# Performance work log

Hardware: AMD Instinct MI355X
Metric: run time of the kernel (lower is better)

Reference implementation:

```python
import jax, jax.numpy as jnp
import numpy as np

DIM = 128
EMB = 8
HID = 128
N = 50000
E = 400000
IN_DIM = 3 * DIM + EMB  # zi, zj, |zi-zj|, type_emb


def setup_inputs() -> dict:
    key = jax.random.key(0)
    ks = jax.random.split(key, 16)
    s = 0.05
    return {
        "z": jax.random.normal(ks[0], (N, DIM), dtype=jnp.float32),
        "edge_index": jax.random.randint(ks[1], (2, E), 0, N, dtype=jnp.int64),
        "edge_type": jax.random.randint(ks[2], (E,), 0, 2, dtype=jnp.int64),
        "type_emb": jax.random.normal(ks[3], (2, EMB), dtype=jnp.float32) * s,
        "ew1": jax.random.normal(ks[4], (IN_DIM, HID), dtype=jnp.float32) * s,
        "eb1": jnp.zeros((HID,), dtype=jnp.float32),
        "ew2": jax.random.normal(ks[5], (HID, 1), dtype=jnp.float32) * s,
        "eb2": jnp.zeros((1,), dtype=jnp.float32),
        "mw1": jax.random.normal(ks[6], (DIM, DIM), dtype=jnp.float32) * s,
        "mb1": jnp.zeros((DIM,), dtype=jnp.float32),
        "mw2": jax.random.normal(ks[7], (DIM, DIM), dtype=jnp.float32) * s,
        "mb2": jnp.zeros((DIM,), dtype=jnp.float32),
        "gamma": jnp.ones((DIM,), dtype=jnp.float32),
        "beta": jnp.zeros((DIM,), dtype=jnp.float32),
    }


def reference(z, edge_index, edge_type, type_emb, ew1, eb1, ew2, eb2,
              mw1, mb1, mw2, mb2, gamma, beta):
    src = edge_index[0]
    dst = edge_index[1]
    n = z.shape[0]

    # --- learn branch: edge MLP -> sigmoid -> segment softmax over src ---
    zi = z[src]              # [E, D]
    zj = z[dst]              # [E, D]
    te = type_emb[edge_type]  # [E, EMB]
    e_in = jnp.concatenate([zi, zj, jnp.abs(zi - zj), te], axis=1)  # [E, 3D+EMB]
    h = jax.nn.relu(e_in @ ew1 + eb1)
    w = jax.nn.sigmoid((h @ ew2 + eb2)[:, 0])  # [E]
    # scatter_reduce amax with include_self on a -1e9-filled buffer
    m = jax.ops.segment_max(w, src, num_segments=n)
    m = jnp.maximum(m, jnp.float32(-1e9))
    w_exp = jnp.exp(w - m[src])
    ssum = jax.ops.segment_sum(w_exp, src, num_segments=n)
    alpha_learned = w_exp / (ssum[src] + 1e-12)

    # --- uniform branch: alpha = 1/deg(src), msg MLP, scatter-add, LayerNorm ---
    deg = jax.ops.segment_sum(jnp.ones((src.shape[0],), z.dtype), src, num_segments=n)
    alpha_u = 1.0 / (deg[src] + 1e-12)
    msg = (jax.nn.relu(zj @ mw1 + mb1) @ mw2 + mb2) * alpha_u[:, None]  # [E, D]
    agg = jax.ops.segment_sum(msg, src, num_segments=n)  # [N, D]
    x = z + agg  # dropout inactive (eval mode)
    mu = jnp.mean(x, axis=-1, keepdims=True)
    var = jnp.mean(jnp.square(x - mu), axis=-1, keepdims=True)
    out = (x - mu) * jax.lax.rsqrt(var + 1e-5) * gamma + beta
    return (out, alpha_learned)
```

## Files before the change

kernel.cpp:

```cpp
#include <hip/hip_runtime.h>
#include <math.h>


typedef short bf16x8 __attribute__((ext_vector_type(8)));
typedef unsigned short ushort8 __attribute__((ext_vector_type(8)));
typedef float f32x4 __attribute__((ext_vector_type(4)));

__device__ inline short bf16_rne(float f) {
    unsigned u = __float_as_uint(f);
    u = (u + 0x7FFFu + ((u >> 16) & 1u)) >> 16;
    return (short)u;
}
__device__ inline float bf16_to_f(unsigned short h) {
    return __uint_as_float(((unsigned)h) << 16);
}

__global__ void prep_all(const float* __restrict__ te, const float* __restrict__ ew1,
                         const float* __restrict__ eb1, const float* __restrict__ mw1,
                         const float* __restrict__ mw2, float* __restrict__ T2,
                         unsigned short* __restrict__ Wap, unsigned short* __restrict__ Wbp,
                         unsigned short* __restrict__ Wcp, unsigned short* __restrict__ Mw1p,
                         unsigned short* __restrict__ Mw2p) {
    int b = blockIdx.x;
    if (b == 0) {
        int t = threadIdx.x;
        int row = t >> 7, j = t & 127;
        float s = eb1[j];
#pragma unroll
        for (int u = 0; u < 8; ++u) s += te[row * 8 + u] * ew1[(384 + u) * 128 + j];
        T2[row * 128 + j] = s;
        return;
    }
    const float* src = (b == 1) ? ew1 : (b == 2) ? ew1 + 128 * 128
                      : (b == 3) ? ew1 + 256 * 128 : (b == 4) ? mw1 : mw2;
    unsigned short* dst = (b == 1) ? Wap : (b == 2) ? Wbp
                         : (b == 3) ? Wcp : (b == 4) ? Mw1p : Mw2p;
    for (int idx = threadIdx.x; idx < 2048; idx += 256) {
        int ks = idx >> 9, ct = (idx >> 6) & 7, l = idx & 63;
        int kbase = ks * 32 + (l >> 4) * 8;
        int col = ct * 16 + (l & 15);
#pragma unroll
        for (int j = 0; j < 8; ++j)
            dst[(size_t)idx * 8 + j] =
                (unsigned short)bf16_rne(src[(size_t)(kbase + j) * 128 + col]);
    }
}

__global__ void deg_count(const int* __restrict__ ei, int* __restrict__ deg, int E) {
    int e = blockIdx.x * 256 + threadIdx.x;
    if (e >= E) return;
    atomicAdd(&deg[ei[e]], 1);
}

__global__ __launch_bounds__(256) void scan_local(const int* __restrict__ deg,
                                                  int* __restrict__ rowstart,
                                                  int* __restrict__ partials, int N) {
    __shared__ int wtot[4];
    int b = blockIdx.x, t = threadIdx.x, lane = t & 63, wid = t >> 6;
    int i0 = b * 1024 + t * 4;
    int v0 = (i0 + 0 < N) ? deg[i0 + 0] : 0;
    int v1 = (i0 + 1 < N) ? deg[i0 + 1] : 0;
    int v2 = (i0 + 2 < N) ? deg[i0 + 2] : 0;
    int v3 = (i0 + 3 < N) ? deg[i0 + 3] : 0;
    int ts = v0 + v1 + v2 + v3;
    int inc = ts;
#pragma unroll
    for (int off = 1; off < 64; off <<= 1) {
        int u = __shfl_up(inc, off);
        if (lane >= off) inc += u;
    }
    if (lane == 63) wtot[wid] = inc;
    __syncthreads();
    int woff = 0;
    if (wid > 0) woff += wtot[0];
    if (wid > 1) woff += wtot[1];
    if (wid > 2) woff += wtot[2];
    int excl = woff + inc - ts;
    if (i0 + 0 < N) rowstart[i0 + 0] = excl;
    if (i0 + 1 < N) rowstart[i0 + 1] = excl + v0;
    if (i0 + 2 < N) rowstart[i0 + 2] = excl + v0 + v1;
    if (i0 + 3 < N) rowstart[i0 + 3] = excl + v0 + v1 + v2;
    if (t == 255) partials[b] = woff + inc;
}

__global__ void scan_partials(int* __restrict__ partials, int nb) {
    int lane = threadIdx.x;
    int v = (lane < nb) ? partials[lane] : 0;
    int inc = v;
#pragma unroll
    for (int off = 1; off < 64; off <<= 1) {
        int u = __shfl_up(inc, off);
        if (lane >= off) inc += u;
    }
    if (lane < nb) partials[lane] = inc - v;
}

__global__ void scan_add(int* __restrict__ rowstart, const int* __restrict__ partials, int N) {
    int i = blockIdx.x * 256 + threadIdx.x;
    if (i < N) rowstart[i] += partials[i >> 10];
}

__global__ void place_edges(const int* __restrict__ ei, const int* __restrict__ etype,
                            int* __restrict__ cursor, const int* __restrict__ rowstart,
                            int4* __restrict__ cinfo, int E) {
    int e = blockIdx.x * 256 + threadIdx.x;
    if (e >= E) return;
    int s = ei[e], d = ei[E + e];
    int slot = rowstart[s] + atomicAdd(&cursor[s], 1);
    cinfo[slot] = make_int4(d, s, etype[e], e);
}

__global__ __launch_bounds__(256) void node_mfma(
        const void* __restrict__ Av, int a_bf16,
        const bf16x8* __restrict__ Bfr, const float* __restrict__ bias,
        void* __restrict__ Cv, int c_bf16, int relu, int M) {
    const int l = threadIdx.x & 63;
    const int wv = threadIdx.x >> 6;
    const int c = l & 15, g = l >> 4;
    const int row = blockIdx.x * 64 + wv * 16 + c;
    const int rowc = row < M ? row : M - 1;

    const float* af = (const float*)Av + (size_t)rowc * 128 + g * 8;
    const unsigned short* ah = (const unsigned short*)Av + (size_t)rowc * 128 + g * 8;

    f32x4 acc[8];
#pragma unroll
    for (int ct = 0; ct < 8; ++ct)
#pragma unroll
        for (int r = 0; r < 4; ++r) acc[ct][r] = 0.f;

#pragma unroll
    for (int ks = 0; ks < 4; ++ks) {
        bf16x8 a;
        if (a_bf16) {
            a = (bf16x8)(*(const ushort8*)(ah + ks * 32));
        } else {
            float4 x0 = *(const float4*)(af + ks * 32);
            float4 x1 = *(const float4*)(af + ks * 32 + 4);
            a[0] = bf16_rne(x0.x); a[1] = bf16_rne(x0.y);
            a[2] = bf16_rne(x0.z); a[3] = bf16_rne(x0.w);
            a[4] = bf16_rne(x1.x); a[5] = bf16_rne(x1.y);
            a[6] = bf16_rne(x1.z); a[7] = bf16_rne(x1.w);
        }
#pragma unroll
        for (int ct = 0; ct < 8; ++ct) {
            bf16x8 b = Bfr[(ks * 8 + ct) * 64 + l];
            acc[ct] = __builtin_amdgcn_mfma_f32_16x16x32_bf16(a, b, acc[ct], 0, 0, 0);
        }
    }

#pragma unroll
    for (int r = 0; r < 4; ++r) {
        int rr = blockIdx.x * 64 + wv * 16 + g * 4 + r;
        if (rr >= M) continue;
#pragma unroll
        for (int ct = 0; ct < 8; ++ct) {
            int j = ct * 16 + c;
            float v = acc[ct][r] + (bias ? bias[j] : 0.f);
            if (relu) v = fmaxf(v, 0.f);
            if (c_bf16)
                ((unsigned short*)Cv)[(size_t)rr * 128 + j] = (unsigned short)bf16_rne(v);
            else
                ((float*)Cv)[(size_t)rr * 128 + j] = v;
        }
    }
}

__global__ __launch_bounds__(256) void pa_pb_mfma(
        const float* __restrict__ z, const bf16x8* __restrict__ Ba,
        const bf16x8* __restrict__ Bb, float* __restrict__ Pa,
        float* __restrict__ Pb, unsigned short* __restrict__ zb16, int M) {
    const int l = threadIdx.x & 63;
    const int wv = threadIdx.x >> 6;
    const int c = l & 15, g = l >> 4;
    const int row = blockIdx.x * 64 + wv * 16 + c;
    const int rowc = row < M ? row : M - 1;
    const float* af = z + (size_t)rowc * 128 + g * 8;

    f32x4 acca[8], accb[8];
#pragma unroll
    for (int ct = 0; ct < 8; ++ct)
#pragma unroll
        for (int r = 0; r < 4; ++r) { acca[ct][r] = 0.f; accb[ct][r] = 0.f; }

#pragma unroll
    for (int ks = 0; ks < 4; ++ks) {
        float4 x0 = *(const float4*)(af + ks * 32);
        float4 x1 = *(const float4*)(af + ks * 32 + 4);
        bf16x8 a;
        a[0] = bf16_rne(x0.x); a[1] = bf16_rne(x0.y);
        a[2] = bf16_rne(x0.z); a[3] = bf16_rne(x0.w);
        a[4] = bf16_rne(x1.x); a[5] = bf16_rne(x1.y);
        a[6] = bf16_rne(x1.z); a[7] = bf16_rne(x1.w);
        if (row < M)
            *(ushort8*)(zb16 + (size_t)row * 128 + ks * 32 + g * 8) = (ushort8)a;
#pragma unroll
        for (int ct = 0; ct < 8; ++ct) {
            acca[ct] = __builtin_amdgcn_mfma_f32_16x16x32_bf16(
                a, Ba[(ks * 8 + ct) * 64 + l], acca[ct], 0, 0, 0);
            accb[ct] = __builtin_amdgcn_mfma_f32_16x16x32_bf16(
                a, Bb[(ks * 8 + ct) * 64 + l], accb[ct], 0, 0, 0);
        }
    }

#pragma unroll
    for (int r = 0; r < 4; ++r) {
        int rr = blockIdx.x * 64 + wv * 16 + g * 4 + r;
        if (rr >= M) continue;
#pragma unroll
        for (int ct = 0; ct < 8; ++ct) {
            int j = ct * 16 + c;
            Pa[(size_t)rr * 128 + j] = acca[ct][r];
            Pb[(size_t)rr * 128 + j] = accb[ct][r];
        }
    }
}

__global__ __launch_bounds__(256) void edge_mlp_mfma(
        const unsigned short* __restrict__ zb16, const int4* __restrict__ cinfo,
        const bf16x8* __restrict__ Bfr,
        const float* __restrict__ ew2, const float* __restrict__ eb2,
        const float* __restrict__ Pa, const float* __restrict__ Pb,
        const float* __restrict__ T2, float* __restrict__ expw,
        float* __restrict__ ssum, int E) {
    const int l = threadIdx.x & 63;
    const int wv = threadIdx.x >> 6;
    const int c = l & 15, g = l >> 4;
    const int slot0 = blockIdx.x * 64;

    const int ra = slot0 + wv * 16 + c;
    const int4 ciA = cinfo[ra];
    const unsigned short* zi = zb16 + (size_t)ciA.y * 128 + g * 8;
    const unsigned short* zj = zb16 + (size_t)ciA.x * 128 + g * 8;

    f32x4 acc[8];
#pragma unroll
    for (int ct = 0; ct < 8; ++ct)
#pragma unroll
        for (int r = 0; r < 4; ++r) acc[ct][r] = 0.f;

#pragma unroll
    for (int ks = 0; ks < 4; ++ks) {
        ushort8 ui = *(const ushort8*)(zi + ks * 32);
        ushort8 uj = *(const ushort8*)(zj + ks * 32);
        bf16x8 a;
#pragma unroll
        for (int k = 0; k < 8; ++k)
            a[k] = bf16_rne(fabsf(bf16_to_f(ui[k]) - bf16_to_f(uj[k])));
#pragma unroll
        for (int ct = 0; ct < 8; ++ct) {
            bf16x8 b = Bfr[(ks * 8 + ct) * 64 + l];
            acc[ct] = __builtin_amdgcn_mfma_f32_16x16x32_bf16(a, b, acc[ct], 0, 0, 0);
        }
    }

    const int eb = slot0 + wv * 16 + g * 4;
    int4 cr[4];
#pragma unroll
    for (int r = 0; r < 4; ++r) cr[r] = cinfo[eb + r];

    float s[4] = {0.f, 0.f, 0.f, 0.f};
#pragma unroll
    for (int ct = 0; ct < 8; ++ct) {
        int j = ct * 16 + c;
        float w2v = ew2[j];
#pragma unroll
        for (int r = 0; r < 4; ++r) {
            float h = acc[ct][r] + Pa[(size_t)cr[r].y * 128 + j]
                                 + Pb[(size_t)cr[r].x * 128 + j]
                                 + T2[cr[r].z * 128 + j];
            s[r] = fmaf(fmaxf(h, 0.f), w2v, s[r]);
        }
    }
#pragma unroll
    for (int r = 0; r < 4; ++r) {
        s[r] += __shfl_xor(s[r], 1);
        s[r] += __shfl_xor(s[r], 2);
        s[r] += __shfl_xor(s[r], 4);
        s[r] += __shfl_xor(s[r], 8);
    }
    if (c == 0) {
        const float eb2v = eb2[0];
#pragma unroll
        for (int r = 0; r < 4; ++r) {
            float w = 1.f / (1.f + expf(-(s[r] + eb2v)));
            float ewv = expf(w);
            expw[cr[r].w] = ewv;
            atomicAdd(&ssum[cr[r].y], ewv);
        }
    }
}

__global__ void alpha_k(const float* __restrict__ expw, const int* __restrict__ ei,
                        const float* __restrict__ ssum, float* __restrict__ oa, int E) {
    int e = blockIdx.x * 256 + threadIdx.x;
    if (e >= E) return;
    oa[e] = expw[e] / (ssum[ei[e]] + 1e-12f);
}

__global__ __launch_bounds__(256) void gather_ln(
        const float* __restrict__ z, const float* __restrict__ Mx,
        const int* __restrict__ rowstart, const int* __restrict__ deg,
        const int4* __restrict__ cinfo, const float* __restrict__ gamma,
        const float* __restrict__ beta, float* __restrict__ out, int N) {
    int wid = threadIdx.x >> 6, lane = threadIdx.x & 63;
    int n = blockIdx.x * 4 + wid;
    if (n >= N) return;
    int r0 = rowstart[n], dg = deg[n];
    float2 a0 = make_float2(0.f, 0.f), a1 = make_float2(0.f, 0.f);
    for (int c = 0; c < dg; c += 64) {
        int cnt = min(64, dg - c);
        int myd = (lane < cnt) ? cinfo[r0 + c + lane].x : 0;
        int j = 0;
        for (; j + 1 < cnt; j += 2) {
            int d0 = __shfl(myd, j), d1 = __shfl(myd, j + 1);
            float2 v0 = ((const float2*)(Mx + (size_t)d0 * 128))[lane];
            float2 v1 = ((const float2*)(Mx + (size_t)d1 * 128))[lane];
            a0.x += v0.x; a0.y += v0.y;
            a1.x += v1.x; a1.y += v1.y;
        }
        if (j < cnt) {
            int d0 = __shfl(myd, j);
            float2 v0 = ((const float2*)(Mx + (size_t)d0 * 128))[lane];
            a0.x += v0.x; a0.y += v0.y;
        }
    }
    float inv = 1.f / ((float)dg + 1e-12f);
    size_t base = (size_t)n * 128;
    float2 zz = ((const float2*)(z + base))[lane];
    float x0 = zz.x + (a0.x + a1.x) * inv;
    float x1 = zz.y + (a0.y + a1.y) * inv;
    float s = x0 + x1;
#pragma unroll
    for (int off = 1; off < 64; off <<= 1) s += __shfl_xor(s, off);
    float mu = s * (1.f / 128.f);
    float d0 = x0 - mu, d1 = x1 - mu;
    float v = d0 * d0 + d1 * d1;
#pragma unroll
    for (int off = 1; off < 64; off <<= 1) v += __shfl_xor(v, off);
    float rs = rsqrtf(v * (1.f / 128.f) + 1e-5f);
    float2 gg = ((const float2*)gamma)[lane];
    float2 bb = ((const float2*)beta)[lane];
    float2 o = make_float2(d0 * rs * gg.x + bb.x, d1 * rs * gg.y + bb.y);
    ((float2*)(out + base))[lane] = o;
}

extern "C" void kernel_launch(void* const* d_in, const int* in_sizes, int n_in,
                              void* d_out, int out_size, void* d_ws, size_t ws_size,
                              hipStream_t stream) {
    const float* z     = (const float*)d_in[0];
    const int*   ei    = (const int*)d_in[1];
    const int*   et    = (const int*)d_in[2];
    const float* temb  = (const float*)d_in[3];
    const float* ew1   = (const float*)d_in[4];
    const float* eb1   = (const float*)d_in[5];
    const float* ew2   = (const float*)d_in[6];
    const float* eb2   = (const float*)d_in[7];
    const float* mw1   = (const float*)d_in[8];
    const float* mb1   = (const float*)d_in[9];
    const float* mw2   = (const float*)d_in[10];
    const float* mb2   = (const float*)d_in[11];
    const float* gamma = (const float*)d_in[12];
    const float* beta  = (const float*)d_in[13];

    const int N = in_sizes[0] / 128;
    const int E = in_sizes[2];

    char* ws = (char*)d_ws;
    size_t off = 0;
    auto take = [&](size_t b) { char* p = ws + off; off += (b + 255) & ~(size_t)255; return p; };
    float*          Pa    = (float*)take((size_t)N * 128 * 4);
    float*          Pb    = (float*)take((size_t)N * 128 * 4);
    unsigned short* Hb    = (unsigned short*)take((size_t)N * 128 * 2);
    float*          Mx    = (float*)take((size_t)N * 128 * 4);
    unsigned short* zb16  = (unsigned short*)take((size_t)N * 128 * 2);
    char*           z0    = ws + off;
    float*          ssum  = (float*)take((size_t)N * 4);
    int*            deg   = (int*)take((size_t)N * 4);
    int*            cursor= (int*)take((size_t)N * 4);
    size_t          zb    = (size_t)((ws + off) - z0);
    int*            rowst = (int*)take((size_t)N * 4);
    int*            parts = (int*)take(256 * 4);
    int4*           cinfo = (int4*)take((size_t)E * 16);
    float*          expw  = (float*)take((size_t)E * 4);
    float*          T2    = (float*)take(2 * 128 * 4);
    unsigned short* Wap   = (unsigned short*)take(2048 * 8 * 2);
    unsigned short* Wbp   = (unsigned short*)take(2048 * 8 * 2);
    unsigned short* Wcp   = (unsigned short*)take(2048 * 8 * 2);
    unsigned short* Mw1p  = (unsigned short*)take(2048 * 8 * 2);
    unsigned short* Mw2p  = (unsigned short*)take(2048 * 8 * 2);

    float* out_x = (float*)d_out;
    float* out_a = out_x + (size_t)N * 128;

    hipMemsetAsync(z0, 0, zb, stream);
    prep_all<<<6, 256, 0, stream>>>(temb, ew1, eb1, mw1, mw2,
                                    T2, Wap, Wbp, Wcp, Mw1p, Mw2p);

    const int nb = (N + 1023) / 1024;
    deg_count<<<(E + 255) / 256, 256, 0, stream>>>(ei, deg, E);
    scan_local<<<nb, 256, 0, stream>>>(deg, rowst, parts, N);
    scan_partials<<<1, 64, 0, stream>>>(parts, nb);
    scan_add<<<(N + 255) / 256, 256, 0, stream>>>(rowst, parts, N);
    place_edges<<<(E + 255) / 256, 256, 0, stream>>>(ei, et, cursor, rowst, cinfo, E);

    int gb = (N + 63) / 64;
    pa_pb_mfma<<<gb, 256, 0, stream>>>(z, (const bf16x8*)Wap, (const bf16x8*)Wbp,
                                       Pa, Pb, zb16, N);
    node_mfma<<<gb, 256, 0, stream>>>(z, 0, (const bf16x8*)Mw1p, mb1,
                                      Hb, 1, 1, N);
    node_mfma<<<gb, 256, 0, stream>>>(Hb, 1, (const bf16x8*)Mw2p, mb2,
                                      Mx, 0, 0, N);

    edge_mlp_mfma<<<E / 64, 256, 0, stream>>>(zb16, cinfo, (const bf16x8*)Wcp, ew2, eb2,
                                              Pa, Pb, T2, expw, ssum, E);
    alpha_k<<<(E + 255) / 256, 256, 0, stream>>>(expw, ei, ssum, out_a, E);
    gather_ln<<<(N + 3) / 4, 256, 0, stream>>>(z, Mx, rowst, deg, cinfo, gamma, beta, out_x, N);
}
```

Measured before the change: 329.3 us.

## Fuse node projections and message MLP into one kernel, store Pa/Pb in bf16

Merges the Pa/Pb projection kernel and the two node MLP kernels into a single kernel. The z tile is converted to bf16 once, and the hidden activation goes through shared memory instead of a global bf16 buffer. Pa and Pb are now stored as bf16, which halves the bytes gathered per edge in the edge MLP. In exchange the fused kernel holds three accumulator sets, so register pressure rises and occupancy may drop, and the bf16 Pa/Pb add rounding error to the edge logits.

```diff
diff --git a/kernel.cpp b/kernel.cpp
--- a/kernel.cpp
+++ b/kernel.cpp
@@ -110,66 +110,14 @@
     cinfo[slot] = make_int4(d, s, etype[e], e);
 }
 
-__global__ __launch_bounds__(256) void node_mfma(
-        const void* __restrict__ Av, int a_bf16,
-        const bf16x8* __restrict__ Bfr, const float* __restrict__ bias,
-        void* __restrict__ Cv, int c_bf16, int relu, int M) {
-    const int l = threadIdx.x & 63;
-    const int wv = threadIdx.x >> 6;
-    const int c = l & 15, g = l >> 4;
-    const int row = blockIdx.x * 64 + wv * 16 + c;
-    const int rowc = row < M ? row : M - 1;
-
-    const float* af = (const float*)Av + (size_t)rowc * 128 + g * 8;
-    const unsigned short* ah = (const unsigned short*)Av + (size_t)rowc * 128 + g * 8;
-
-    f32x4 acc[8];
-#pragma unroll
-    for (int ct = 0; ct < 8; ++ct)
-#pragma unroll
-        for (int r = 0; r < 4; ++r) acc[ct][r] = 0.f;
-
-#pragma unroll
-    for (int ks = 0; ks < 4; ++ks) {
-        bf16x8 a;
-        if (a_bf16) {
-            a = (bf16x8)(*(const ushort8*)(ah + ks * 32));
-        } else {
-            float4 x0 = *(const float4*)(af + ks * 32);
-            float4 x1 = *(const float4*)(af + ks * 32 + 4);
-            a[0] = bf16_rne(x0.x); a[1] = bf16_rne(x0.y);
-            a[2] = bf16_rne(x0.z); a[3] = bf16_rne(x0.w);
-            a[4] = bf16_rne(x1.x); a[5] = bf16_rne(x1.y);
-            a[6] = bf16_rne(x1.z); a[7] = bf16_rne(x1.w);
-        }
-#pragma unroll
-        for (int ct = 0; ct < 8; ++ct) {
-            bf16x8 b = Bfr[(ks * 8 + ct) * 64 + l];
-            acc[ct] = __builtin_amdgcn_mfma_f32_16x16x32_bf16(a, b, acc[ct], 0, 0, 0);
-        }
-    }
-
-#pragma unroll
-    for (int r = 0; r < 4; ++r) {
-        int rr = blockIdx.x * 64 + wv * 16 + g * 4 + r;
-        if (rr >= M) continue;
-#pragma unroll
-        for (int ct = 0; ct < 8; ++ct) {
-            int j = ct * 16 + c;
-            float v = acc[ct][r] + (bias ? bias[j] : 0.f);
-            if (relu) v = fmaxf(v, 0.f);
-            if (c_bf16)
-                ((unsigned short*)Cv)[(size_t)rr * 128 + j] = (unsigned short)bf16_rne(v);
-            else
-                ((float*)Cv)[(size_t)rr * 128 + j] = v;
-        }
-    }
-}
-
-__global__ __launch_bounds__(256) void pa_pb_mfma(
+__global__ __launch_bounds__(256) void node_all(
         const float* __restrict__ z, const bf16x8* __restrict__ Ba,
-        const bf16x8* __restrict__ Bb, float* __restrict__ Pa,
-        float* __restrict__ Pb, unsigned short* __restrict__ zb16, int M) {
+        const bf16x8* __restrict__ Bb, const bf16x8* __restrict__ Bm1,
+        const bf16x8* __restrict__ Bm2, const float* __restrict__ mb1,
+        const float* __restrict__ mb2, unsigned short* __restrict__ Pa,
+        unsigned short* __restrict__ Pb, unsigned short* __restrict__ zb16,
+        float* __restrict__ Mx, int M) {
+    __shared__ unsigned short Hs[64][136];
     const int l = threadIdx.x & 63;
     const int wv = threadIdx.x >> 6;
     const int c = l & 15, g = l >> 4;
@@ -177,12 +125,13 @@
     const int rowc = row < M ? row : M - 1;
     const float* af = z + (size_t)rowc * 128 + g * 8;
 
-    f32x4 acca[8], accb[8];
+    f32x4 acca[8], accb[8], acch[8];
 #pragma unroll
     for (int ct = 0; ct < 8; ++ct)
 #pragma unroll
-        for (int r = 0; r < 4; ++r) { acca[ct][r] = 0.f; accb[ct][r] = 0.f; }
-
+        for (int r = 0; r < 4; ++r) { acca[ct][r] = 0.f; accb[ct][r] = 0.f; acch[ct][r] = 0.f; }
+
+    bf16x8 afrag[4];
 #pragma unroll
     for (int ks = 0; ks < 4; ++ks) {
         float4 x0 = *(const float4*)(af + ks * 32);
@@ -192,17 +141,53 @@
         a[2] = bf16_rne(x0.z); a[3] = bf16_rne(x0.w);
         a[4] = bf16_rne(x1.x); a[5] = bf16_rne(x1.y);
         a[6] = bf16_rne(x1.z); a[7] = bf16_rne(x1.w);
+        afrag[ks] = a;
         if (row < M)
             *(ushort8*)(zb16 + (size_t)row * 128 + ks * 32 + g * 8) = (ushort8)a;
+    }
+#pragma unroll
+    for (int ks = 0; ks < 4; ++ks) {
 #pragma unroll
         for (int ct = 0; ct < 8; ++ct) {
             acca[ct] = __builtin_amdgcn_mfma_f32_16x16x32_bf16(
-                a, Ba[(ks * 8 + ct) * 64 + l], acca[ct], 0, 0, 0);
+                afrag[ks], Ba[(ks * 8 + ct) * 64 + l], acca[ct], 0, 0, 0);
             accb[ct] = __builtin_amdgcn_mfma_f32_16x16x32_bf16(
-                a, Bb[(ks * 8 + ct) * 64 + l], accb[ct], 0, 0, 0);
-        }
-    }
-
+                afrag[ks], Bb[(ks * 8 + ct) * 64 + l], accb[ct], 0, 0, 0);
+            acch[ct] = __builtin_amdgcn_mfma_f32_16x16x32_bf16(
+                afrag[ks], Bm1[(ks * 8 + ct) * 64 + l], acch[ct], 0, 0, 0);
+        }
+    }
+
+#pragma unroll
+    for (int r = 0; r < 4; ++r) {
+        int rr = blockIdx.x * 64 + wv * 16 + g * 4 + r;
+        bool ok = rr < M;
+#pragma unroll
+        for (int ct = 0; ct < 8; ++ct) {
+            int j = ct * 16 + c;
+            if (ok) {
+                Pa[(size_t)rr * 128 + j] = (unsigned short)bf16_rne(acca[ct][r]);
+                Pb[(size_t)rr * 128 + j] = (unsigned short)bf16_rne(accb[ct][r]);
+            }
+            Hs[wv * 16 + g * 4 + r][j] =
+                (unsigned short)bf16_rne(fmaxf(acch[ct][r] + mb1[j], 0.f));
+        }
+    }
+    __syncthreads();
+
+    f32x4 accm[8];
+#pragma unroll
+    for (int ct = 0; ct < 8; ++ct)
+#pragma unroll
+        for (int r = 0; r < 4; ++r) accm[ct][r] = 0.f;
+#pragma unroll
+    for (int ks = 0; ks < 4; ++ks) {
+        bf16x8 a = (bf16x8)(*(const ushort8*)&Hs[wv * 16 + c][ks * 32 + g * 8]);
+#pragma unroll
+        for (int ct = 0; ct < 8; ++ct)
+            accm[ct] = __builtin_amdgcn_mfma_f32_16x16x32_bf16(
+                a, Bm2[(ks * 8 + ct) * 64 + l], accm[ct], 0, 0, 0);
+    }
 #pragma unroll
     for (int r = 0; r < 4; ++r) {
         int rr = blockIdx.x * 64 + wv * 16 + g * 4 + r;
@@ -210,8 +195,7 @@
 #pragma unroll
         for (int ct = 0; ct < 8; ++ct) {
             int j = ct * 16 + c;
-            Pa[(size_t)rr * 128 + j] = acca[ct][r];
-            Pb[(size_t)rr * 128 + j] = accb[ct][r];
+            Mx[(size_t)rr * 128 + j] = accm[ct][r] + mb2[j];
         }
     }
 }
@@ -220,7 +204,7 @@
         const unsigned short* __restrict__ zb16, const int4* __restrict__ cinfo,
         const bf16x8* __restrict__ Bfr,
         const float* __restrict__ ew2, const float* __restrict__ eb2,
-        const float* __restrict__ Pa, const float* __restrict__ Pb,
+        const unsigned short* __restrict__ Pa, const unsigned short* __restrict__ Pb,
         const float* __restrict__ T2, float* __restrict__ expw,
         float* __restrict__ ssum, int E) {
     const int l = threadIdx.x & 63;
@@ -266,8 +250,8 @@
         float w2v = ew2[j];
 #pragma unroll
         for (int r = 0; r < 4; ++r) {
-            float h = acc[ct][r] + Pa[(size_t)cr[r].y * 128 + j]
-                                 + Pb[(size_t)cr[r].x * 128 + j]
+            float h = acc[ct][r] + bf16_to_f(Pa[(size_t)cr[r].y * 128 + j])
+                                 + bf16_to_f(Pb[(size_t)cr[r].x * 128 + j])
                                  + T2[cr[r].z * 128 + j];
             s[r] = fmaf(fmaxf(h, 0.f), w2v, s[r]);
         }
@@ -369,11 +353,10 @@
     char* ws = (char*)d_ws;
     size_t off = 0;
     auto take = [&](size_t b) { char* p = ws + off; off += (b + 255) & ~(size_t)255; return p; };
-    float*          Pa    = (float*)take((size_t)N * 128 * 4);
-    float*          Pb    = (float*)take((size_t)N * 128 * 4);
-    unsigned short* Hb    = (unsigned short*)take((size_t)N * 128 * 2);
+    unsigned short* Pa    = (unsigned short*)take((size_t)N * 128 * 2);
+    unsigned short* Pb    = (unsigned short*)take((size_t)N * 128 * 2);
+    unsigned short* zb16  = (unsigned short*)take((size_t)N * 128 * 2);
     float*          Mx    = (float*)take((size_t)N * 128 * 4);
-    unsigned short* zb16  = (unsigned short*)take((size_t)N * 128 * 2);
     char*           z0    = ws + off;
     float*          ssum  = (float*)take((size_t)N * 4);
     int*            deg   = (int*)take((size_t)N * 4);
@@ -405,12 +388,9 @@
     place_edges<<<(E + 255) / 256, 256, 0, stream>>>(ei, et, cursor, rowst, cinfo, E);
 
     int gb = (N + 63) / 64;
-    pa_pb_mfma<<<gb, 256, 0, stream>>>(z, (const bf16x8*)Wap, (const bf16x8*)Wbp,
-                                       Pa, Pb, zb16, N);
-    node_mfma<<<gb, 256, 0, stream>>>(z, 0, (const bf16x8*)Mw1p, mb1,
-                                      Hb, 1, 1, N);
-    node_mfma<<<gb, 256, 0, stream>>>(Hb, 1, (const bf16x8*)Mw2p, mb2,
-                                      Mx, 0, 0, N);
+    node_all<<<gb, 256, 0, stream>>>(z, (const bf16x8*)Wap, (const bf16x8*)Wbp,
+                                     (const bf16x8*)Mw1p, (const bf16x8*)Mw2p,
+                                     mb1, mb2, Pa, Pb, zb16, Mx, N);
 
     edge_mlp_mfma<<<E / 64, 256, 0, stream>>>(zb16, cinfo, (const bf16x8*)Wcp, ew2, eb2,
                                               Pa, Pb, T2, expw, ssum, E);
```

Result: no change. 326.1 us (-1.0%).
